# Performance work log

Hardware: AMD Instinct MI355X
Metric: run time of the kernel (lower is better)

Reference implementation:

```python
import jax, jax.numpy as jnp
import numpy as np

T, N, D, H = 12, 50000, 32, 128  # timesteps, nodes, input_dim, hidden_dim
DEC_STEPS = 7


def setup_inputs() -> dict:
    key = jax.random.key(0)
    ks = jax.random.split(key, 10)
    w = lambda k, shape, s=0.1: jax.random.normal(k, shape, dtype=jnp.float32) * s
    return {
        "x": jax.random.normal(ks[0], (T, N, D), dtype=jnp.float32),
        # input_encoder: Linear(D, H)
        "enc_W": w(ks[1], (H, D)), "enc_b": jnp.zeros((H,), jnp.float32),
        # encoder LSTM (1 layer), PyTorch gate order i,f,g,o
        "Wih_e": w(ks[2], (4 * H, H)), "Whh_e": w(ks[3], (4 * H, H)),
        "bih_e": jnp.zeros((4 * H,), jnp.float32), "bhh_e": jnp.zeros((4 * H,), jnp.float32),
        # decoder LSTM (1 layer)
        "Wih_d": w(ks[4], (4 * H, H)), "Whh_d": w(ks[5], (4 * H, H)),
        "bih_d": jnp.zeros((4 * H,), jnp.float32), "bhh_d": jnp.zeros((4 * H,), jnp.float32),
        # head: fc1(H -> H//2), fc2(H//2 -> 1)
        "fc1_W": w(ks[6], (H // 2, H)), "fc1_b": jnp.zeros((H // 2,), jnp.float32),
        "fc2_W": w(ks[7], (1, H // 2)), "fc2_b": jnp.zeros((1,), jnp.float32),
    }


def _lstm_cell(x, h, c, Wih, Whh, b):
    # PyTorch LSTM gate layout: [i, f, g, o] along the 4H axis.
    z = x @ Wih.T + h @ Whh.T + b
    i, f, g, o = jnp.split(z, 4, axis=-1)
    c = jax.nn.sigmoid(f) * c + jax.nn.sigmoid(i) * jnp.tanh(g)
    h = jax.nn.sigmoid(o) * jnp.tanh(c)
    return h, c


def reference(x, enc_W, enc_b, Wih_e, Whh_e, bih_e, bhh_e,
              Wih_d, Whh_d, bih_d, bhh_d, fc1_W, fc1_b, fc2_W, fc2_b):
    t, n, d = x.shape
    h_dim = enc_W.shape[0]
    # input_encoder applied to all nodes/timesteps at once: [T,N,H]
    enc_seq = jax.nn.relu(jnp.einsum('tnd,hd->tnh', x, enc_W) + enc_b)

    h0 = jnp.zeros((n, h_dim), x.dtype)
    c0 = jnp.zeros((n, h_dim), x.dtype)
    b_e = bih_e + bhh_e

    def enc_step(carry, xt):
        h, c = carry
        h, c = _lstm_cell(xt, h, c, Wih_e, Whh_e, b_e)
        return (h, c), None

    (h, c), _ = jax.lax.scan(enc_step, (h0, c0), enc_seq)

    # decoder input = last encoder output (fixed across all 7 steps, as in source)
    d_in = h
    b_d = bih_d + bhh_d

    def dec_step(carry, _):
        hd, cd = carry
        hd, cd = _lstm_cell(d_in, hd, cd, Wih_d, Whh_d, b_d)
        out = jax.nn.relu(hd @ fc1_W.T + fc1_b)  # dropout is identity at inference
        pred = out @ fc2_W.T + fc2_b             # [N, 1]
        return (hd, cd), pred[:, 0]

    _, preds = jax.lax.scan(dec_step, (h, c), None, length=DEC_STEPS)  # [7, N]
    return preds.T  # [N, 7]
```

## Files before the change

kernel.cpp:

```cpp
#include <hip/hip_runtime.h>

#define TSTEPS 12
#define NNODES 50000
#define DIN 32
#define HDIM 128
#define DECS 7

#define N80 53
#define NB 768
#define RTMAX 5
#define ROWSMAX 80

#define HS 136
#define XS 36
#define ESZ (ROWSMAX * HS)

typedef _Float16 half_t;
typedef _Float16 half8 __attribute__((ext_vector_type(8)));
typedef float float4_ __attribute__((ext_vector_type(4)));

#define WS_FLOAT_OFF 548864

#define SM_BYTES 157440
#define E_OFF 69120
#define H_OFF 112640
#define PRED_OFF 156160
#define ZX_PLANE_H 20480

#if __has_builtin(__builtin_amdgcn_exp2f)
#define EXP2F __builtin_amdgcn_exp2f
#else
#define EXP2F exp2f
#endif
#if __has_builtin(__builtin_amdgcn_rcpf)
#define RCPF __builtin_amdgcn_rcpf
#else
#define RCPF(x) (1.0f / (x))
#endif

__device__ __forceinline__ float lstm_one(float zi, float zf, float zg, float zo, float& c) {
    float ai = EXP2F(-zi);
    float af = EXP2F(-zf);
    float ag = EXP2F(-zg);
    float ao = EXP2F(-zo);
    float sf = RCPF(1.0f + af);
    float tg = 1.0f + ag;
    float ig = (1.0f - ag) * RCPF(fmaf(ai, tg, tg));
    c = fmaf(sf, c, ig);
    float ac = EXP2F(-2.88539008f * c);
    float tc = 1.0f + ac;
    return (1.0f - ac) * RCPF(fmaf(ao, tc, tc));
}

__global__ void prep_all_k(const float* __restrict__ Wih_e, const float* __restrict__ Whh_e,
                           const float* __restrict__ Wih_d, const float* __restrict__ Whh_d,
                           const float* __restrict__ enc_W, const float* __restrict__ fc1_W,
                           const float* __restrict__ bih_e, const float* __restrict__ bhh_e,
                           const float* __restrict__ bih_d, const float* __restrict__ bhh_d,
                           half_t* __restrict__ wsh, float* __restrict__ be, float* __restrict__ bd) {
    int tid = blockIdx.x * blockDim.x + threadIdx.x;
    if (tid < 262144) {
        int r = tid >> 16;
        int t = tid & 65535;
        const float* src = (r == 0) ? Wih_e : (r == 1) ? Whh_e : (r == 2) ? Wih_d : Whh_d;
        int j    = t & 7;
        int lane = (t >> 3) & 63;
        int rest = t >> 9;
        int kb   = rest & 3;
        int ct   = rest >> 2;
        int row  = ct * 16 + (lane & 15);
        int col  = kb * 32 + ((lane >> 4) << 3) + j;
        float scl = ((ct >> 3) == 2) ? 2.8853900818f : 1.4426950409f;
        wsh[tid] = (half_t)(src[row * 128 + col] * scl);
    } else if (tid < 266240) {
        int t    = tid - 262144;
        int j    = t & 7;
        int lane = (t >> 3) & 63;
        int ct   = t >> 9;
        int row  = ct * 16 + (lane & 15);
        int col  = ((lane >> 4) << 3) + j;
        wsh[tid] = (half_t)enc_W[row * 32 + col];
    } else if (tid < 274432) {
        int t    = tid - 266240;
        int j    = t & 7;
        int lane = (t >> 3) & 63;
        int rest = t >> 9;
        int kb   = rest & 3;
        int ct   = rest >> 2;
        int row  = ct * 16 + (lane & 15);
        int col  = kb * 32 + ((lane >> 4) << 3) + j;
        wsh[tid] = (half_t)fc1_W[row * 128 + col];
    } else if (tid < 274944) {
        int t = tid - 274432;
        float scl = ((t >> 7) == 2) ? 2.8853900818f : 1.4426950409f;
        be[t] = (bih_e[t] + bhh_e[t]) * scl;
        bd[t] = (bih_d[t] + bhh_d[t]) * scl;
    }
}

__device__ __forceinline__ void lstm_step(
    const half_t* __restrict__ eA, const half_t* __restrict__ hA, half_t* __restrict__ hOut,
    const half8 (&wfA)[4][4], const half8 (&wfB)[4][4],
    const float bR[4], float (&cS)[RTMAX][4],
    int w, int q, int l15, int RT) {
#pragma unroll
    for (int rt = 0; rt < RTMAX; ++rt) {
        if (rt < RT) {
            float4_ acc[4];
#pragma unroll
            for (int g = 0; g < 4; ++g) {
                float b = bR[g];
                acc[g][0] = b; acc[g][1] = b; acc[g][2] = b; acc[g][3] = b;
            }
            __builtin_amdgcn_s_setprio(1);
#pragma unroll
            for (int kb = 0; kb < 4; ++kb) {
                half8 ae = *(const half8*)(eA + (rt * 16 + l15) * HS + kb * 32 + q * 8);
                half8 ah = *(const half8*)(hA + (rt * 16 + l15) * HS + kb * 32 + q * 8);
#pragma unroll
                for (int g = 0; g < 4; ++g) {
                    acc[g] = __builtin_amdgcn_mfma_f32_16x16x32_f16(ae, wfA[g][kb], acc[g], 0, 0, 0);
                    acc[g] = __builtin_amdgcn_mfma_f32_16x16x32_f16(ah, wfB[g][kb], acc[g], 0, 0, 0);
                }
            }
            __builtin_amdgcn_s_setprio(0);
#pragma unroll
            for (int r = 0; r < 4; ++r) {
                float h = lstm_one(acc[0][r], acc[1][r], acc[2][r], acc[3][r], cS[rt][r]);
                hOut[(rt * 16 + q * 4 + r) * HS + w * 16 + l15] = (half_t)h;
            }
        }
    }
}

__device__ __forceinline__ void lstm_step_dec(
    const half_t* __restrict__ zx, const half_t* __restrict__ hA, half_t* __restrict__ hOut,
    const half8 (&wfh)[4][4], float (&cS)[RTMAX][4],
    int w, int q, int l15, int lane, int RT) {
#pragma unroll
    for (int rt = 0; rt < RTMAX; ++rt) {
        if (rt < RT) {
            const half_t* p0 = zx + ((w * RTMAX + rt) * 64 + lane) * 8;
            half8 z0 = *(const half8*)p0;
            half8 z1 = *(const half8*)(p0 + ZX_PLANE_H);
            float4_ acc[4];
#pragma unroll
            for (int r = 0; r < 4; ++r) {
                acc[0][r] = (float)z0[r];
                acc[1][r] = (float)z0[4 + r];
                acc[2][r] = (float)z1[r];
                acc[3][r] = (float)z1[4 + r];
            }
            __builtin_amdgcn_s_setprio(1);
#pragma unroll
            for (int kb = 0; kb < 4; ++kb) {
                half8 ah = *(const half8*)(hA + (rt * 16 + l15) * HS + kb * 32 + q * 8);
#pragma unroll
                for (int g = 0; g < 4; ++g)
                    acc[g] = __builtin_amdgcn_mfma_f32_16x16x32_f16(ah, wfh[g][kb], acc[g], 0, 0, 0);
            }
            __builtin_amdgcn_s_setprio(0);
#pragma unroll
            for (int r = 0; r < 4; ++r) {
                float h = lstm_one(acc[0][r], acc[1][r], acc[2][r], acc[3][r], cS[rt][r]);
                hOut[(rt * 16 + q * 4 + r) * HS + w * 16 + l15] = (half_t)h;
            }
        }
    }
}

__device__ __forceinline__ void enc_proj(
    const half_t* __restrict__ xa, half_t* __restrict__ eOut,
    half8 encWf, float benc, int t, int w, int q, int l15, int RT) {
#pragma unroll
    for (int rt = 0; rt < RTMAX; ++rt) {
        if (rt < RT) {
            half8 af = *(const half8*)(xa + ((t * ROWSMAX) + rt * 16 + l15) * XS + q * 8);
            float4_ a;
            a[0] = benc; a[1] = benc; a[2] = benc; a[3] = benc;
            a = __builtin_amdgcn_mfma_f32_16x16x32_f16(af, encWf, a, 0, 0, 0);
#pragma unroll
            for (int r = 0; r < 4; ++r) {
                float v = a[r];
                v = v > 0.f ? v : 0.f;
                eOut[(rt * 16 + q * 4 + r) * HS + w * 16 + l15] = (half_t)v;
            }
        }
    }
}

__global__ __launch_bounds__(512, 2) void seq2seq_main_k(
    const float* __restrict__ x,
    const float* __restrict__ enc_b,
    const float* __restrict__ fc1_b,
    const float* __restrict__ fc2_W,
    const float* __restrict__ fc2_b,
    const half_t* __restrict__ wsh,
    const float* __restrict__ be,
    const float* __restrict__ bd,
    float* __restrict__ out) {
    __shared__ __align__(16) char smem[SM_BYTES];
    half_t* xa = (half_t*)smem;
    half_t* eB = (half_t*)(smem + E_OFF);
    half_t* hB = (half_t*)(smem + H_OFF);
    float (*pred)[ROWSMAX] = (float(*)[ROWSMAX])(smem + PRED_OFF);
    half_t* zx = (half_t*)smem;

    const int tid  = threadIdx.x;
    const int lane = tid & 63;
    const int w    = tid >> 6;
    const int q    = lane >> 4;
    const int l15  = lane & 15;
    const int ph   = (w >> 2) & 1;
    const int bid  = blockIdx.x;
    const int big  = (bid < N80);
    const int RT   = big ? 5 : 4;
    const int rows = RT << 4;
    const int n0   = big ? bid * 80 : (N80 * 80 + (bid - N80) * 64);

    const half_t* WihE  = wsh;
    const half_t* WhhE  = wsh + 65536;
    const half_t* WihD  = wsh + 131072;
    const half_t* WhhD  = wsh + 196608;
    const half_t* encWp = wsh + 262144;
    const half_t* fc1p  = wsh + 266240;

    float beR[4], bdR[4];
#pragma unroll
    for (int g = 0; g < 4; ++g) {
        int col = g * 128 + w * 16 + l15;
        beR[g] = be[col];
        bdR[g] = bd[col];
    }
    float benc = enc_b[w * 16 + l15];

    for (int it = 0; it < 8; ++it) {
        int unit = tid + it * 512;
        if (unit >= TSTEPS * ROWSMAX * 4) break;
        int t    = unit / (ROWSMAX * 4);
        int rest = unit - t * (ROWSMAX * 4);
        int row  = rest >> 2;
        int c0   = (rest & 3) * 8;
        if (row < rows) {
            const float* p = x + ((size_t)t * NNODES + (n0 + row)) * DIN + c0;
            float4_ a0 = *(const float4_*)p;
            float4_ a1 = *(const float4_*)(p + 4);
            half8 hv;
            hv[0] = (half_t)a0[0]; hv[1] = (half_t)a0[1]; hv[2] = (half_t)a0[2]; hv[3] = (half_t)a0[3];
            hv[4] = (half_t)a1[0]; hv[5] = (half_t)a1[1]; hv[6] = (half_t)a1[2]; hv[7] = (half_t)a1[3];
            *(half8*)(xa + (t * ROWSMAX + row) * XS + c0) = hv;
        }
    }

    for (int i = tid; i < rows * HS; i += 512) hB[i] = (half_t)0.0f;

    float c_reg[RTMAX][4];
#pragma unroll
    for (int rt = 0; rt < RTMAX; ++rt)
#pragma unroll
        for (int r = 0; r < 4; ++r) c_reg[rt][r] = 0.0f;

    half8 wfi[4][4], wfh[4][4];
#pragma unroll
    for (int g = 0; g < 4; ++g)
#pragma unroll
        for (int kb = 0; kb < 4; ++kb) {
            int ct = g * 8 + w;
            wfi[g][kb] = *(const half8*)(WihE + ((size_t)(ct * 4 + kb) * 64 + lane) * 8);
            wfh[g][kb] = *(const half8*)(WhhE + ((size_t)(ct * 4 + kb) * 64 + lane) * 8);
        }
    half8 encWf = *(const half8*)(encWp + (size_t)w * 512 + lane * 8);

    __syncthreads();

    enc_proj(xa, eB, encWf, benc, 0, w, q, l15, RT);
    __syncthreads();

    int cur = 0;
    for (int t = 0; t < TSTEPS; ++t) {
        const half_t* eCur  = eB + (t & 1) * ESZ;
        half_t*       eNext = eB + ((t & 1) ^ 1) * ESZ;
        const half_t* hCur  = hB + cur * ESZ;
        half_t*       hNext = hB + (cur ^ 1) * ESZ;
        if (!ph) {
            lstm_step(eCur, hCur, hNext, wfi, wfh, beR, c_reg, w, q, l15, RT);
            if (t + 1 < TSTEPS)
                enc_proj(xa, eNext, encWf, benc, t + 1, w, q, l15, RT);
        } else {
            if (t + 1 < TSTEPS)
                enc_proj(xa, eNext, encWf, benc, t + 1, w, q, l15, RT);
            lstm_step(hCur, eCur, hNext, wfh, wfi, beR, c_reg, w, q, l15, RT);
        }
        __syncthreads();
        cur ^= 1;
    }

#pragma unroll
    for (int g = 0; g < 4; ++g)
#pragma unroll
        for (int kb = 0; kb < 4; ++kb) {
            int ct = g * 8 + w;
            wfi[g][kb] = *(const half8*)(WihD + ((size_t)(ct * 4 + kb) * 64 + lane) * 8);
            wfh[g][kb] = *(const half8*)(WhhD + ((size_t)(ct * 4 + kb) * 64 + lane) * 8);
        }
    half8 fc1f[4];
#pragma unroll
    for (int kb = 0; kb < 4; ++kb)
        fc1f[kb] = *(const half8*)(fc1p + ((size_t)((w & 3) * 4 + kb) * 64 + lane) * 8);
    float bf1 = fc1_b[(w & 3) * 16 + l15];
    float wf2 = fc2_W[(w & 3) * 16 + l15];
    float bf2 = fc2_b[0];
    const int gg = w >> 2;

    {
        const half_t* hfin = hB + cur * ESZ;
#pragma unroll
        for (int rt = 0; rt < RTMAX; ++rt) {
            if (rt < RT) {
                float4_ acc[4];
#pragma unroll
                for (int g = 0; g < 4; ++g) {
                    float b = bdR[g];
                    acc[g][0] = b; acc[g][1] = b; acc[g][2] = b; acc[g][3] = b;
                }
#pragma unroll
                for (int kb = 0; kb < 4; ++kb) {
                    half8 ah = *(const half8*)(hfin + (rt * 16 + l15) * HS + kb * 32 + q * 8);
#pragma unroll
                    for (int g = 0; g < 4; ++g)
                        acc[g] = __builtin_amdgcn_mfma_f32_16x16x32_f16(ah, wfi[g][kb], acc[g], 0, 0, 0);
                }
                half8 z0, z1;
#pragma unroll
                for (int r = 0; r < 4; ++r) {
                    z0[r]     = (half_t)acc[0][r];
                    z0[4 + r] = (half_t)acc[1][r];
                    z1[r]     = (half_t)acc[2][r];
                    z1[4 + r] = (half_t)acc[3][r];
                }
                half_t* p0 = zx + ((w * RTMAX + rt) * 64 + lane) * 8;
                *(half8*)p0 = z0;
                *(half8*)(p0 + ZX_PLANE_H) = z1;
            }
        }
    }

    for (int s = 0; s < DECS; ++s) {
        lstm_step_dec(zx, hB + cur * ESZ, hB + (cur ^ 1) * ESZ, wfh, c_reg, w, q, l15, lane, RT);
        cur ^= 1;
        __syncthreads();
        const half_t* hc = hB + cur * ESZ;
#pragma unroll
        for (int rp = 0; rp < 3; ++rp) {
            int rt = gg + rp * 2;
            if (rt < RT) {
                float4_ hacc;
                hacc[0] = bf1; hacc[1] = bf1; hacc[2] = bf1; hacc[3] = bf1;
#pragma unroll
                for (int kb = 0; kb < 4; ++kb) {
                    half8 af = *(const half8*)(hc + (rt * 16 + l15) * HS + kb * 32 + q * 8);
                    hacc = __builtin_amdgcn_mfma_f32_16x16x32_f16(af, fc1f[kb], hacc, 0, 0, 0);
                }
#pragma unroll
                for (int r = 0; r < 4; ++r) {
                    float v = hacc[r];
                    v = v > 0.f ? v : 0.f;
                    v *= wf2;
                    v += __shfl_xor(v, 1, 64);
                    v += __shfl_xor(v, 2, 64);
                    v += __shfl_xor(v, 4, 64);
                    v += __shfl_xor(v, 8, 64);
                    if (l15 == 0) pred[w & 3][rt * 16 + q * 4 + r] = v;
                }
            }
        }
        __syncthreads();
        if (tid < rows) {
            float sum = pred[0][tid] + pred[1][tid] + pred[2][tid] + pred[3][tid] + bf2;
            out[(size_t)(n0 + tid) * DECS + s] = sum;
        }
    }
}

extern "C" void kernel_launch(void* const* d_in, const int* in_sizes, int n_in,
                              void* d_out, int out_size, void* d_ws, size_t ws_size,
                              hipStream_t stream) {
    (void)in_sizes; (void)n_in; (void)out_size; (void)ws_size;
    const float* x     = (const float*)d_in[0];
    const float* enc_W = (const float*)d_in[1];
    const float* enc_b = (const float*)d_in[2];
    const float* Wih_e = (const float*)d_in[3];
    const float* Whh_e = (const float*)d_in[4];
    const float* bih_e = (const float*)d_in[5];
    const float* bhh_e = (const float*)d_in[6];
    const float* Wih_d = (const float*)d_in[7];
    const float* Whh_d = (const float*)d_in[8];
    const float* bih_d = (const float*)d_in[9];
    const float* bhh_d = (const float*)d_in[10];
    const float* fc1_W = (const float*)d_in[11];
    const float* fc1_b = (const float*)d_in[12];
    const float* fc2_W = (const float*)d_in[13];
    const float* fc2_b = (const float*)d_in[14];

    half_t* wsh = (half_t*)d_ws;
    float*  be  = (float*)((char*)d_ws + WS_FLOAT_OFF);
    float*  bd  = be + 512;

    prep_all_k<<<1074, 256, 0, stream>>>(Wih_e, Whh_e, Wih_d, Whh_d, enc_W, fc1_W,
                                         bih_e, bhh_e, bih_d, bhh_d, wsh, be, bd);

    seq2seq_main_k<<<NB, 512, 0, stream>>>(x, enc_b, fc1_b, fc2_W, fc2_b,
                                           wsh, be, bd, (float*)d_out);
}
```

Before: 397.6 us.

## Software-pipeline decoder head with LSTM steps and fold cell-state math

The decoder loop now runs the fc1/fc2 head for the previous step and reduces the step before that inside the same barrier interval as the next LSTM step. This uses double-buffered pred arrays and cuts the barriers per decoder step from two to one. The LSTM cell update is also rewritten to merge the forget and input gate reciprocals into a single reciprocal, and the cell state is kept pre-scaled by 2/ln2 to drop a multiply. It costs a slightly larger shared-memory footprint and changes rounding in the cell-state computation.

```diff
diff --git a/kernel.cpp b/kernel.cpp
--- a/kernel.cpp
+++ b/kernel.cpp
@@ -21,7 +21,7 @@
 
 #define WS_FLOAT_OFF 548864
 
-#define SM_BYTES 157440
+#define SM_BYTES 158720
 #define E_OFF 69120
 #define H_OFF 112640
 #define PRED_OFF 156160
@@ -38,16 +38,18 @@
 #define RCPF(x) (1.0f / (x))
 #endif
 
-__device__ __forceinline__ float lstm_one(float zi, float zf, float zg, float zo, float& c) {
+__device__ __forceinline__ float lstm_one(float zi, float zf, float zg, float zo, float& cp) {
     float ai = EXP2F(-zi);
     float af = EXP2F(-zf);
     float ag = EXP2F(-zg);
     float ao = EXP2F(-zo);
-    float sf = RCPF(1.0f + af);
+    float D1 = 1.0f + af;
     float tg = 1.0f + ag;
-    float ig = (1.0f - ag) * RCPF(fmaf(ai, tg, tg));
-    c = fmaf(sf, c, ig);
-    float ac = EXP2F(-2.88539008f * c);
+    float D2 = fmaf(ai, tg, tg);
+    float M  = fmaf(ag, -2.8853900818f, 2.8853900818f);
+    float num = fmaf(M, D1, cp * D2);
+    cp = num * RCPF(D1 * D2);
+    float ac = EXP2F(-cp);
     float tc = 1.0f + ac;
     return (1.0f - ac) * RCPF(fmaf(ao, tc, tc));
 }
@@ -189,6 +191,36 @@
     }
 }
 
+__device__ __forceinline__ void head_step(
+    const half_t* __restrict__ hc, float (*pred)[ROWSMAX],
+    const half8 (&fc1f)[4], float bf1, float wf2,
+    int w, int q, int l15, int gg, int RT) {
+#pragma unroll
+    for (int rp = 0; rp < 3; ++rp) {
+        int rt = gg + rp * 2;
+        if (rt < RT) {
+            float4_ hacc;
+            hacc[0] = bf1; hacc[1] = bf1; hacc[2] = bf1; hacc[3] = bf1;
+#pragma unroll
+            for (int kb = 0; kb < 4; ++kb) {
+                half8 af = *(const half8*)(hc + (rt * 16 + l15) * HS + kb * 32 + q * 8);
+                hacc = __builtin_amdgcn_mfma_f32_16x16x32_f16(af, fc1f[kb], hacc, 0, 0, 0);
+            }
+#pragma unroll
+            for (int r = 0; r < 4; ++r) {
+                float v = hacc[r];
+                v = v > 0.f ? v : 0.f;
+                v *= wf2;
+                v += __shfl_xor(v, 1, 64);
+                v += __shfl_xor(v, 2, 64);
+                v += __shfl_xor(v, 4, 64);
+                v += __shfl_xor(v, 8, 64);
+                if (l15 == 0) pred[w & 3][rt * 16 + q * 4 + r] = v;
+            }
+        }
+    }
+}
+
 __global__ __launch_bounds__(512, 2) void seq2seq_main_k(
     const float* __restrict__ x,
     const float* __restrict__ enc_b,
@@ -203,7 +235,7 @@
     half_t* xa = (half_t*)smem;
     half_t* eB = (half_t*)(smem + E_OFF);
     half_t* hB = (half_t*)(smem + H_OFF);
-    float (*pred)[ROWSMAX] = (float(*)[ROWSMAX])(smem + PRED_OFF);
+    float (*pred)[4][ROWSMAX] = (float(*)[4][ROWSMAX])(smem + PRED_OFF);
     half_t* zx = (half_t*)smem;
 
     const int tid  = threadIdx.x;
@@ -345,40 +377,28 @@
         }
     }
 
+    int hc = cur;
     for (int s = 0; s < DECS; ++s) {
-        lstm_step_dec(zx, hB + cur * ESZ, hB + (cur ^ 1) * ESZ, wfh, c_reg, w, q, l15, lane, RT);
-        cur ^= 1;
+        lstm_step_dec(zx, hB + hc * ESZ, hB + (hc ^ 1) * ESZ, wfh, c_reg, w, q, l15, lane, RT);
+        if (s >= 1)
+            head_step(hB + hc * ESZ, pred[(s - 1) & 1], fc1f, bf1, wf2, w, q, l15, gg, RT);
+        if (s >= 2 && tid < rows) {
+            float sum = pred[s & 1][0][tid] + pred[s & 1][1][tid]
+                      + pred[s & 1][2][tid] + pred[s & 1][3][tid] + bf2;
+            out[(size_t)(n0 + tid) * DECS + (s - 2)] = sum;
+        }
         __syncthreads();
-        const half_t* hc = hB + cur * ESZ;
-#pragma unroll
-        for (int rp = 0; rp < 3; ++rp) {
-            int rt = gg + rp * 2;
-            if (rt < RT) {
-                float4_ hacc;
-                hacc[0] = bf1; hacc[1] = bf1; hacc[2] = bf1; hacc[3] = bf1;
-#pragma unroll
-                for (int kb = 0; kb < 4; ++kb) {
-                    half8 af = *(const half8*)(hc + (rt * 16 + l15) * HS + kb * 32 + q * 8);
-                    hacc = __builtin_amdgcn_mfma_f32_16x16x32_f16(af, fc1f[kb], hacc, 0, 0, 0);
-                }
-#pragma unroll
-                for (int r = 0; r < 4; ++r) {
-                    float v = hacc[r];
-                    v = v > 0.f ? v : 0.f;
-                    v *= wf2;
-                    v += __shfl_xor(v, 1, 64);
-                    v += __shfl_xor(v, 2, 64);
-                    v += __shfl_xor(v, 4, 64);
-                    v += __shfl_xor(v, 8, 64);
-                    if (l15 == 0) pred[w & 3][rt * 16 + q * 4 + r] = v;
-                }
-            }
-        }
-        __syncthreads();
-        if (tid < rows) {
-            float sum = pred[0][tid] + pred[1][tid] + pred[2][tid] + pred[3][tid] + bf2;
-            out[(size_t)(n0 + tid) * DECS + s] = sum;
-        }
+        hc ^= 1;
+    }
+    head_step(hB + hc * ESZ, pred[0], fc1f, bf1, wf2, w, q, l15, gg, RT);
+    if (tid < rows) {
+        float sum = pred[1][0][tid] + pred[1][1][tid] + pred[1][2][tid] + pred[1][3][tid] + bf2;
+        out[(size_t)(n0 + tid) * DECS + 5] = sum;
+    }
+    __syncthreads();
+    if (tid < rows) {
+        float sum = pred[0][0][tid] + pred[0][1][tid] + pred[0][2][tid] + pred[0][3][tid] + bf2;
+        out[(size_t)(n0 + tid) * DECS + 6] = sum;
     }
 }
 
```

Result: faster. 386.9 us (-2.7%).
